# Kernel tuning notes

Hardware: AMD Instinct MI355X
Metric: run time of the kernel (lower is better)

## Reference

```python
import jax, jax.numpy as jnp
import numpy as np

MAX_BLOCK = 4
DOWNSAMPLE = 2
EMBED = 256
VOCAB = 256
BATCH = 16
SEQ = 3072


def sinusoidal_pe(max_len, d):
    pos = np.arange(max_len, dtype=np.float32)[:, None]
    div = np.exp(np.arange(0, d, 2, dtype=np.float32) * (-np.log(10000.0) / d))
    pe = np.zeros((max_len, d), dtype=np.float32)
    pe[:, 0::2] = np.sin(pos * div)
    pe[:, 1::2] = np.cos(pos * div)
    return jnp.asarray(pe)


def avg_pool_ceil(x, k):
    # x: [B, L, H], kernel=stride=k, ceil_mode=True (partial last window divides by valid count)
    B, L, H = x.shape
    S = -(-L // k)
    pad = S * k - L
    xp = jnp.pad(x, ((0, 0), (0, pad), (0, 0)))
    sums = xp.reshape(B, S, k, H).sum(axis=2)
    counts = jnp.minimum(k, L - jnp.arange(S) * k).astype(x.dtype)
    return sums / counts[None, :, None]


def setup_inputs() -> dict:
    key = jax.random.key(0)
    k1, k2, k3 = jax.random.split(key, 3)
    input_ids = jax.random.randint(k1, (BATCH, SEQ), 0, VOCAB)
    embed_table = jax.random.normal(k2, (VOCAB, EMBED), dtype=jnp.float32) * 0.02
    embed_table = embed_table.at[0].set(0.0)  # padding_idx=0
    w_score = jax.random.normal(k3, (1, EMBED), dtype=jnp.float32) * 0.02
    b_score = jnp.zeros((1,), dtype=jnp.float32)
    return {"input_ids": input_ids, "embed_table": embed_table,
            "w_score": w_score, "b_score": b_score}


def reference(input_ids, embed_table, w_score, b_score):
    B, L = input_ids.shape
    H = embed_table.shape[1]
    emb = embed_table[input_ids]  # [B, L, H]

    # positional encoding with period MAX_BLOCK, tiled over the sequence
    pe = sinusoidal_pe(MAX_BLOCK, H)  # [MAX_BLOCK, H]
    reps = L // MAX_BLOCK + 1
    pe_t = jnp.tile(pe, (reps, 1))[:L]  # [L, H]
    x = emb + pe_t[None, :, :]  # same positioned embedding used for every block size

    Xs = []
    Sc = []
    for bs in range(1, MAX_BLOCK + 1):
        pooled = avg_pool_ceil(x, bs)                 # [B, S, H]
        sc = pooled @ w_score.T + b_score             # [B, S, 1]
        Xs.append(jnp.repeat(pooled, bs, axis=1)[:, :L, :])   # [B, L, H]
        Sc.append(jnp.repeat(sc[..., 0], bs, axis=1)[:, :L])  # [B, L]

    scores = jax.nn.softmax(jnp.stack(Sc, axis=-1), axis=-1)  # [B, L, M]
    s = scores[..., None]                                      # [B, L, M, 1]
    # score calibration: softmax(s s^T) @ s over tiny MxM
    attn = jax.nn.softmax(s @ jnp.swapaxes(s, -1, -2), axis=-1)  # [B, L, M, M]
    s = (attn @ s)[..., 0]                                        # [B, L, M]

    X = jnp.stack(Xs, axis=0)  # [M, B, L, H]
    combined = jnp.einsum('mblh,blm->blh', X, s)  # [B, L, H]

    # downsample avg pool over length (ceil mode; L divisible so exact)
    out = avg_pool_ceil(combined, DOWNSAMPLE)  # [B, L/DOWNSAMPLE, H]
    return out
```

## Files before the change

kernel.cpp:

```cpp
#include <hip/hip_runtime.h>
#include <math.h>


#define BATCH   16
#define SEQ     3072
#define EMBED   256
#define CHUNK   48
#define OUTROWS 24
#define NCHUNK  (SEQ / CHUNK)
#define OUTL    (SEQ / 2)

__device__ inline float4 f4add(float4 a, float4 b) {
    return make_float4(a.x + b.x, a.y + b.y, a.z + b.z, a.w + b.w);
}
__device__ inline float4 f4fma(float4 acc, float s, float4 a) {
    acc.x += s * a.x; acc.y += s * a.y; acc.z += s * a.z; acc.w += s * a.w;
    return acc;
}

__global__ __launch_bounds__(256) void gbst_kernel(
        const int* __restrict__ ids, const float* __restrict__ E,
        const float* __restrict__ w, const float* __restrict__ b_score,
        float* __restrict__ out) {
    __shared__ float4 x_s[CHUNK * 64];
    __shared__ float4 pe_s4[4 * 64];
    __shared__ float4 w_s4[64];
    __shared__ int    id_s[CHUNK];
    __shared__ float  y_s[CHUNK];
    __shared__ float4 c_s[CHUNK];

    const int tid   = threadIdx.x;
    const int b     = blockIdx.x >> 6;
    const int chunk = blockIdx.x & 63;
    const int pos0  = chunk * CHUNK;
    const int wave  = tid >> 6, lane = tid & 63;

    if (tid < CHUNK) id_s[tid] = ids[b * SEQ + pos0 + tid];
    ((float*)w_s4)[tid] = w[tid];

    {
        float* pe_sf = (float*)pe_s4;
        const int i = tid >> 1;
        const float div = expf((float)(2 * i) * -0.03597789207803197f);
        #pragma unroll
        for (int q = 0; q < 4; ++q) {
            const float ang = (float)q * div;
            pe_sf[q * EMBED + tid] = (tid & 1) ? cosf(ang) : sinf(ang);
        }
    }
    __syncthreads();

    const float4* E4 = (const float4*)E;
    #pragma unroll
    for (int k = 0; k < 12; ++k) {
        const int t = k * 4 + wave;
        const float4 e = E4[id_s[t] * 64 + lane];
        const float4 p = pe_s4[(t & 3) * 64 + lane];
        const float4 x = f4add(e, p);
        x_s[t * 64 + lane] = x;
        const float4 ww = w_s4[lane];
        float d = x.x * ww.x + x.y * ww.y + x.z * ww.z + x.w * ww.w;
        #pragma unroll
        for (int off = 32; off > 0; off >>= 1) d += __shfl_down(d, off);
        if (lane == 0) y_s[t] = d;
    }
    __syncthreads();

    if (tid < CHUNK) {
        const int l = tid;
        const float bsc = b_score[0];
        const float m1 = y_s[l];
        const int l2 = l & ~1;
        const float m2 = 0.5f * (y_s[l2] + y_s[l2 + 1]);
        const int l3 = (l / 3) * 3;
        const float m3 = (1.f / 3.f) * (y_s[l3] + y_s[l3 + 1] + y_s[l3 + 2]);
        const int l4 = l & ~3;
        const float m4 = 0.25f * (y_s[l4] + y_s[l4+1] + y_s[l4+2] + y_s[l4+3]);

        float sc[4] = {m1 + bsc, m2 + bsc, m3 + bsc, m4 + bsc};
        float mx = fmaxf(fmaxf(sc[0], sc[1]), fmaxf(sc[2], sc[3]));
        float p[4], sum = 0.f;
        #pragma unroll
        for (int m = 0; m < 4; ++m) { p[m] = expf(sc[m] - mx); sum += p[m]; }
        const float inv = 1.f / sum;
        #pragma unroll
        for (int m = 0; m < 4; ++m) p[m] *= inv;

        float snew[4];
        #pragma unroll
        for (int i = 0; i < 4; ++i) {
            const float q0 = p[i]*p[0], q1 = p[i]*p[1], q2 = p[i]*p[2], q3 = p[i]*p[3];
            const float mq = fmaxf(fmaxf(q0, q1), fmaxf(q2, q3));
            const float e0 = expf(q0 - mq), e1 = expf(q1 - mq),
                        e2 = expf(q2 - mq), e3 = expf(q3 - mq);
            snew[i] = (e0*p[0] + e1*p[1] + e2*p[2] + e3*p[3]) / (e0+e1+e2+e3);
        }
        c_s[l] = make_float4(snew[0], snew[1] * 0.5f,
                             snew[2] * (1.f / 3.f), snew[3] * 0.25f);
    }
    __syncthreads();

    #pragma unroll
    for (int k = 0; k < 6; ++k) {
        const int r  = wave * 6 + k;
        const int l0 = 2 * r, l1 = l0 + 1;

        const float4 x0 = x_s[l0 * 64 + lane];
        const float4 x1 = x_s[l1 * 64 + lane];
        const float4 S2 = f4add(x0, x1);

        const int b4 = l0 & ~3;
        const float4 S4 = f4add(f4add(x_s[b4*64 + lane], x_s[(b4+1)*64 + lane]),
                                f4add(x_s[(b4+2)*64 + lane], x_s[(b4+3)*64 + lane]));

        const int j3a = l0 / 3, j3b = l1 / 3;
        const int t3a = 3 * j3a;
        const float4 S3a = f4add(f4add(x_s[t3a*64 + lane], x_s[(t3a+1)*64 + lane]),
                                 x_s[(t3a+2)*64 + lane]);
        float4 S3b = S3a;
        if (j3b != j3a) {
            const int t3b = 3 * j3b;
            S3b = f4add(f4add(x_s[t3b*64 + lane], x_s[(t3b+1)*64 + lane]),
                        x_s[(t3b+2)*64 + lane]);
        }

        const float4 ca = c_s[l0];
        const float4 cb = c_s[l1];

        float4 acc = make_float4(0.f, 0.f, 0.f, 0.f);
        acc = f4fma(acc, ca.x, x0);
        acc = f4fma(acc, cb.x, x1);
        acc = f4fma(acc, ca.y + cb.y, S2);
        acc = f4fma(acc, ca.z, S3a);
        acc = f4fma(acc, cb.z, S3b);
        acc = f4fma(acc, ca.w + cb.w, S4);
        acc.x *= 0.5f; acc.y *= 0.5f; acc.z *= 0.5f; acc.w *= 0.5f;

        ((float4*)out)[(b * OUTL + chunk * OUTROWS + r) * 64 + lane] = acc;
    }
}

extern "C" void kernel_launch(void* const* d_in, const int* in_sizes, int n_in,
                              void* d_out, int out_size, void* d_ws, size_t ws_size,
                              hipStream_t stream) {
    const int*   ids = (const int*)d_in[0];
    const float* E   = (const float*)d_in[1];
    const float* w   = (const float*)d_in[2];
    const float* bsc = (const float*)d_in[3];
    float*       out = (float*)d_out;

    gbst_kernel<<<BATCH * NCHUNK, 256, 0, stream>>>(ids, E, w, bsc, out);
}
```

Baseline: 82.67 us.

## Process 12-token groups per wavefront entirely in registers without LDS or barriers

Each wavefront now handles an independent group of 12 tokens (an LCM of the block sizes), keeping the embeddings in registers instead of shared memory. Score reductions use xor shuffles so every lane holds all 12 scores, and the per-position softmax weights are broadcast with shuffles. This removes the shared-memory staging and the three block-wide barriers, and computes the positional encoding per lane. In exchange, register pressure rises (48 floats of x plus partial sums) and there are many shuffles per group, with sin/cos recomputed in every wave.

Result: faster. 76.22 us (-7.8%).

```diff
diff --git a/kernel.cpp b/kernel.cpp
--- a/kernel.cpp
+++ b/kernel.cpp
@@ -2,13 +2,13 @@
 #include <math.h>
 
 
-#define BATCH   16
-#define SEQ     3072
-#define EMBED   256
-#define CHUNK   48
-#define OUTROWS 24
-#define NCHUNK  (SEQ / CHUNK)
-#define OUTL    (SEQ / 2)
+#define BATCH 16
+#define SEQ   3072
+#define EMBED 256
+#define OUTL  (SEQ / 2)
+#define GPB   (SEQ / 12)
+#define WPB   4
+#define NBLK  (BATCH * GPB / WPB)
 
 __device__ inline float4 f4add(float4 a, float4 b) {
     return make_float4(a.x + b.x, a.y + b.y, a.z + b.z, a.w + b.w);
@@ -17,126 +17,131 @@
     acc.x += s * a.x; acc.y += s * a.y; acc.z += s * a.z; acc.w += s * a.w;
     return acc;
 }
+__device__ inline float dot4(float4 a, float4 b) {
+    return a.x * b.x + a.y * b.y + a.z * b.z + a.w * b.w;
+}
+
+__device__ inline float sel12(int i, float a0, float a1, float a2, float a3,
+                              float a4, float a5, float a6, float a7,
+                              float a8, float a9, float a10, float a11) {
+    return i == 0 ? a0 : i == 1 ? a1 : i == 2 ? a2 : i == 3 ? a3 :
+           i == 4 ? a4 : i == 5 ? a5 : i == 6 ? a6 : i == 7 ? a7 :
+           i == 8 ? a8 : i == 9 ? a9 : i == 10 ? a10 : a11;
+}
+__device__ inline float sel6(int i, float a0, float a1, float a2,
+                             float a3, float a4, float a5) {
+    return i == 0 ? a0 : i == 1 ? a1 : i == 2 ? a2 :
+           i == 3 ? a3 : i == 4 ? a4 : a5;
+}
+__device__ inline float sel4(int i, float a0, float a1, float a2, float a3) {
+    return i == 0 ? a0 : i == 1 ? a1 : i == 2 ? a2 : a3;
+}
+__device__ inline float sel3(int i, float a0, float a1, float a2) {
+    return i == 0 ? a0 : i == 1 ? a1 : a2;
+}
 
 __global__ __launch_bounds__(256) void gbst_kernel(
         const int* __restrict__ ids, const float* __restrict__ E,
         const float* __restrict__ w, const float* __restrict__ b_score,
         float* __restrict__ out) {
-    __shared__ float4 x_s[CHUNK * 64];
-    __shared__ float4 pe_s4[4 * 64];
-    __shared__ float4 w_s4[64];
-    __shared__ int    id_s[CHUNK];
-    __shared__ float  y_s[CHUNK];
-    __shared__ float4 c_s[CHUNK];
-
-    const int tid   = threadIdx.x;
-    const int b     = blockIdx.x >> 6;
-    const int chunk = blockIdx.x & 63;
-    const int pos0  = chunk * CHUNK;
-    const int wave  = tid >> 6, lane = tid & 63;
-
-    if (tid < CHUNK) id_s[tid] = ids[b * SEQ + pos0 + tid];
-    ((float*)w_s4)[tid] = w[tid];
-
-    {
-        float* pe_sf = (float*)pe_s4;
-        const int i = tid >> 1;
-        const float div = expf((float)(2 * i) * -0.03597789207803197f);
-        #pragma unroll
-        for (int q = 0; q < 4; ++q) {
-            const float ang = (float)q * div;
-            pe_sf[q * EMBED + tid] = (tid & 1) ? cosf(ang) : sinf(ang);
-        }
-    }
-    __syncthreads();
+    const int tid  = threadIdx.x;
+    const int wave = tid >> 6, lane = tid & 63;
+    const int grp  = blockIdx.x * WPB + wave;
+    const int b    = grp >> 8;
+    const int g    = grp & 255;
+    const int pos0 = g * 12;
 
     const float4* E4 = (const float4*)E;
+    const float4 w4  = ((const float4*)w)[lane];
+    const float bias = b_score[0];
+    int idv = 0;
+    if (lane < 12) idv = ids[b * SEQ + pos0 + lane];
+
+    const float c1 = -0.035977892080032f;
+    const float da = expf((float)(4 * lane) * c1);
+    const float db = expf((float)(4 * lane + 2) * c1);
+    const float4 pe1 = make_float4(sinf(da), cosf(da), sinf(db), cosf(db));
+    const float4 pe2 = make_float4(sinf(2.f*da), cosf(2.f*da), sinf(2.f*db), cosf(2.f*db));
+    const float4 pe3 = make_float4(sinf(3.f*da), cosf(3.f*da), sinf(3.f*db), cosf(3.f*db));
+
+    float4 x[12];
     #pragma unroll
-    for (int k = 0; k < 12; ++k) {
-        const int t = k * 4 + wave;
-        const float4 e = E4[id_s[t] * 64 + lane];
-        const float4 p = pe_s4[(t & 3) * 64 + lane];
-        const float4 x = f4add(e, p);
-        x_s[t * 64 + lane] = x;
-        const float4 ww = w_s4[lane];
-        float d = x.x * ww.x + x.y * ww.y + x.z * ww.z + x.w * ww.w;
+    for (int t = 0; t < 12; ++t) {
+        const int idt = __shfl(idv, t);
+        const float4 e = E4[idt * 64 + lane];
+        const float4 p = (t & 3) == 0 ? make_float4(0.f, 1.f, 0.f, 1.f)
+                       : (t & 3) == 1 ? pe1 : (t & 3) == 2 ? pe2 : pe3;
+        x[t] = f4add(e, p);
+    }
+
+    float y[12];
+    #pragma unroll
+    for (int t = 0; t < 12; ++t) {
+        float d = dot4(x[t], w4);
         #pragma unroll
-        for (int off = 32; off > 0; off >>= 1) d += __shfl_down(d, off);
-        if (lane == 0) y_s[t] = d;
+        for (int off = 1; off < 64; off <<= 1) d += __shfl_xor(d, off);
+        y[t] = d;
     }
-    __syncthreads();
 
-    if (tid < CHUNK) {
-        const int l = tid;
-        const float bsc = b_score[0];
-        const float m1 = y_s[l];
-        const int l2 = l & ~1;
-        const float m2 = 0.5f * (y_s[l2] + y_s[l2 + 1]);
-        const int l3 = (l / 3) * 3;
-        const float m3 = (1.f / 3.f) * (y_s[l3] + y_s[l3 + 1] + y_s[l3 + 2]);
-        const int l4 = l & ~3;
-        const float m4 = 0.25f * (y_s[l4] + y_s[l4+1] + y_s[l4+2] + y_s[l4+3]);
+    const float s2_0 = y[0]+y[1],  s2_1 = y[2]+y[3],  s2_2 = y[4]+y[5];
+    const float s2_3 = y[6]+y[7],  s2_4 = y[8]+y[9],  s2_5 = y[10]+y[11];
+    const float s3_0 = y[0]+y[1]+y[2],  s3_1 = y[3]+y[4]+y[5];
+    const float s3_2 = y[6]+y[7]+y[8],  s3_3 = y[9]+y[10]+y[11];
+    const float s4_0 = s2_0+s2_1, s4_1 = s2_2+s2_3, s4_2 = s2_4+s2_5;
 
-        float sc[4] = {m1 + bsc, m2 + bsc, m3 + bsc, m4 + bsc};
-        float mx = fmaxf(fmaxf(sc[0], sc[1]), fmaxf(sc[2], sc[3]));
-        float p[4], sum = 0.f;
-        #pragma unroll
-        for (int m = 0; m < 4; ++m) { p[m] = expf(sc[m] - mx); sum += p[m]; }
-        const float inv = 1.f / sum;
-        #pragma unroll
-        for (int m = 0; m < 4; ++m) p[m] *= inv;
+    const int l = lane;
+    const float m1 = sel12(l, y[0],y[1],y[2],y[3],y[4],y[5],
+                              y[6],y[7],y[8],y[9],y[10],y[11]);
+    const float m2 = 0.5f        * sel6(l >> 1, s2_0,s2_1,s2_2,s2_3,s2_4,s2_5);
+    const float m3 = (1.f/3.f)   * sel4(l / 3, s3_0,s3_1,s3_2,s3_3);
+    const float m4 = 0.25f       * sel3(l >> 2, s4_0,s4_1,s4_2);
 
-        float snew[4];
-        #pragma unroll
-        for (int i = 0; i < 4; ++i) {
-            const float q0 = p[i]*p[0], q1 = p[i]*p[1], q2 = p[i]*p[2], q3 = p[i]*p[3];
-            const float mq = fmaxf(fmaxf(q0, q1), fmaxf(q2, q3));
-            const float e0 = expf(q0 - mq), e1 = expf(q1 - mq),
-                        e2 = expf(q2 - mq), e3 = expf(q3 - mq);
-            snew[i] = (e0*p[0] + e1*p[1] + e2*p[2] + e3*p[3]) / (e0+e1+e2+e3);
-        }
-        c_s[l] = make_float4(snew[0], snew[1] * 0.5f,
-                             snew[2] * (1.f / 3.f), snew[3] * 0.25f);
+    float sc0 = m1 + bias, sc1 = m2 + bias, sc2 = m3 + bias, sc3 = m4 + bias;
+    const float mx = fmaxf(fmaxf(sc0, sc1), fmaxf(sc2, sc3));
+    float p0 = expf(sc0 - mx), p1 = expf(sc1 - mx),
+          p2 = expf(sc2 - mx), p3 = expf(sc3 - mx);
+    const float pinv = 1.f / (p0 + p1 + p2 + p3);
+    p0 *= pinv; p1 *= pinv; p2 *= pinv; p3 *= pinv;
+
+    float sn[4];
+    #pragma unroll
+    for (int i = 0; i < 4; ++i) {
+        const float pi = i == 0 ? p0 : i == 1 ? p1 : i == 2 ? p2 : p3;
+        const float q0 = pi*p0, q1 = pi*p1, q2 = pi*p2, q3 = pi*p3;
+        const float mq = fmaxf(fmaxf(q0, q1), fmaxf(q2, q3));
+        const float e0 = expf(q0-mq), e1 = expf(q1-mq),
+                    e2 = expf(q2-mq), e3 = expf(q3-mq);
+        sn[i] = (e0*p0 + e1*p1 + e2*p2 + e3*p3) / (e0+e1+e2+e3);
     }
-    __syncthreads();
+    const float cc0 = sn[0], cc1 = sn[1]*0.5f, cc2 = sn[2]*(1.f/3.f), cc3 = sn[3]*0.25f;
 
+    float4 T[4], F[3];
+    T[0] = f4add(f4add(x[0], x[1]), x[2]);
+    T[1] = f4add(f4add(x[3], x[4]), x[5]);
+    T[2] = f4add(f4add(x[6], x[7]), x[8]);
+    T[3] = f4add(f4add(x[9], x[10]), x[11]);
+    F[0] = f4add(f4add(x[0], x[1]), f4add(x[2], x[3]));
+    F[1] = f4add(f4add(x[4], x[5]), f4add(x[6], x[7]));
+    F[2] = f4add(f4add(x[8], x[9]), f4add(x[10], x[11]));
+
+    float4* out4 = (float4*)out;
+    const long obase = (long)b * OUTL + g * 6;
     #pragma unroll
-    for (int k = 0; k < 6; ++k) {
-        const int r  = wave * 6 + k;
-        const int l0 = 2 * r, l1 = l0 + 1;
-
-        const float4 x0 = x_s[l0 * 64 + lane];
-        const float4 x1 = x_s[l1 * 64 + lane];
-        const float4 S2 = f4add(x0, x1);
-
-        const int b4 = l0 & ~3;
-        const float4 S4 = f4add(f4add(x_s[b4*64 + lane], x_s[(b4+1)*64 + lane]),
-                                f4add(x_s[(b4+2)*64 + lane], x_s[(b4+3)*64 + lane]));
-
-        const int j3a = l0 / 3, j3b = l1 / 3;
-        const int t3a = 3 * j3a;
-        const float4 S3a = f4add(f4add(x_s[t3a*64 + lane], x_s[(t3a+1)*64 + lane]),
-                                 x_s[(t3a+2)*64 + lane]);
-        float4 S3b = S3a;
-        if (j3b != j3a) {
-            const int t3b = 3 * j3b;
-            S3b = f4add(f4add(x_s[t3b*64 + lane], x_s[(t3b+1)*64 + lane]),
-                        x_s[(t3b+2)*64 + lane]);
-        }
-
-        const float4 ca = c_s[l0];
-        const float4 cb = c_s[l1];
-
+    for (int r = 0; r < 6; ++r) {
+        const int l0 = 2*r, l1 = 2*r + 1;
+        const float ca0 = __shfl(cc0, l0), ca1 = __shfl(cc1, l0),
+                    ca2 = __shfl(cc2, l0), ca3 = __shfl(cc3, l0);
+        const float cb0 = __shfl(cc0, l1), cb1 = __shfl(cc1, l1),
+                    cb2 = __shfl(cc2, l1), cb3 = __shfl(cc3, l1);
         float4 acc = make_float4(0.f, 0.f, 0.f, 0.f);
-        acc = f4fma(acc, ca.x, x0);
-        acc = f4fma(acc, cb.x, x1);
-        acc = f4fma(acc, ca.y + cb.y, S2);
-        acc = f4fma(acc, ca.z, S3a);
-        acc = f4fma(acc, cb.z, S3b);
-        acc = f4fma(acc, ca.w + cb.w, S4);
+        acc = f4fma(acc, ca0, x[l0]);
+        acc = f4fma(acc, cb0, x[l1]);
+        acc = f4fma(acc, ca1 + cb1, f4add(x[l0], x[l1]));
+        acc = f4fma(acc, ca2, T[l0 / 3]);
+        acc = f4fma(acc, cb2, T[l1 / 3]);
+        acc = f4fma(acc, ca3 + cb3, F[r >> 1]);
         acc.x *= 0.5f; acc.y *= 0.5f; acc.z *= 0.5f; acc.w *= 0.5f;
-
-        ((float4*)out)[(b * OUTL + chunk * OUTROWS + r) * 64 + lane] = acc;
+        out4[(obase + r) * 64 + lane] = acc;
     }
 }
 
@@ -149,5 +154,5 @@
     const float* bsc = (const float*)d_in[3];
     float*       out = (float*)d_out;
 
-    gbst_kernel<<<BATCH * NCHUNK, 256, 0, stream>>>(ids, E, w, bsc, out);
+    gbst_kernel<<<NBLK, 256, 0, stream>>>(ids, E, w, bsc, out);
 }
```
